# Kernel tuning notes

Measured on AMD Instinct MI355X. Metric: run time of the kernel, lower is better.

The kernel has to match this reference:

```python
import jax, jax.numpy as jnp
import numpy as np

TEMPERATURE = 8.0  # sqrt(d_k) with d_k = 64

def setup_inputs() -> dict:
    key = jax.random.key(0)
    kq, kk, kv = jax.random.split(key, 3)
    B, L, D = 16, 2048, 64  # heads, seq_len, head_dim
    q = jax.random.normal(kq, (B, L, D), dtype=jnp.float32)
    k = jax.random.normal(kk, (B, L, D), dtype=jnp.float32)
    v = jax.random.normal(kv, (B, L, D), dtype=jnp.float32)
    return {"q": q, "k": k, "v": v}

def reference(q, k, v):
    # scores: [B, Lq, Lk]
    scores = jnp.einsum('bqd,bkd->bqk', q, k) / TEMPERATURE
    log_attn = jax.nn.log_softmax(scores, axis=-1)
    attn = jnp.exp(log_attn)  # softmax, reusing the single stable reduction
    out = jnp.einsum('bqk,bkd->bqd', attn, v)        # [B, Lq, Dv]
    B, Lk, Dv = v.shape
    # transpose(0,1).reshape(Lk, Dv*B): heads folded into feature dim
    output = jnp.transpose(out, (1, 0, 2)).reshape(Lk, Dv * B)
    return (output, attn, log_attn)
```

## Files before the change

kernel.cpp:

```cpp
#include <hip/hip_runtime.h>

#define LSEQ 2048
#define NH   16
#define HD   64

typedef __attribute__((ext_vector_type(8))) short short8;
typedef __attribute__((ext_vector_type(4))) float f32x4;

__device__ __forceinline__ unsigned short f2b(float x) {
  unsigned int u = __builtin_bit_cast(unsigned int, x);
  u += 0x7FFFu + ((u >> 16) & 1u);
  return (unsigned short)(u >> 16);
}

__global__ __launch_bounds__(256) void prep_kernel(
    const float* __restrict__ q, const float* __restrict__ k, const float* __restrict__ v,
    unsigned short* __restrict__ qf, unsigned short* __restrict__ kf,
    unsigned short* __restrict__ vf) {
  const int b = blockIdx.y, lt = blockIdx.x;
  const int t = threadIdx.x;
  __shared__ unsigned short qls[64][80];
  __shared__ unsigned short kls[64][80];
  __shared__ float vls[64][65];
  const int l0 = lt * 64;

  #pragma unroll
  for (int i = 0; i < 2; ++i) {
    int c = t + i * 256;
    int r = c >> 3, d0 = (c & 7) * 8;
    size_t base = ((size_t)(b * LSEQ + l0 + r)) * HD + d0;
    float4 qa = *(const float4*)(q + base);
    float4 qc = *(const float4*)(q + base + 4);
    float4 ka = *(const float4*)(k + base);
    float4 kc = *(const float4*)(k + base + 4);
    float4 va = *(const float4*)(v + base);
    float4 vc = *(const float4*)(v + base + 4);
    qls[r][d0 + 0] = f2b(qa.x * 0.125f); qls[r][d0 + 1] = f2b(qa.y * 0.125f);
    qls[r][d0 + 2] = f2b(qa.z * 0.125f); qls[r][d0 + 3] = f2b(qa.w * 0.125f);
    qls[r][d0 + 4] = f2b(qc.x * 0.125f); qls[r][d0 + 5] = f2b(qc.y * 0.125f);
    qls[r][d0 + 6] = f2b(qc.z * 0.125f); qls[r][d0 + 7] = f2b(qc.w * 0.125f);
    kls[r][d0 + 0] = f2b(ka.x); kls[r][d0 + 1] = f2b(ka.y);
    kls[r][d0 + 2] = f2b(ka.z); kls[r][d0 + 3] = f2b(ka.w);
    kls[r][d0 + 4] = f2b(kc.x); kls[r][d0 + 5] = f2b(kc.y);
    kls[r][d0 + 6] = f2b(kc.z); kls[r][d0 + 7] = f2b(kc.w);
    vls[r][d0 + 0] = va.x; vls[r][d0 + 1] = va.y;
    vls[r][d0 + 2] = va.z; vls[r][d0 + 3] = va.w;
    vls[r][d0 + 4] = vc.x; vls[r][d0 + 5] = vc.y;
    vls[r][d0 + 6] = vc.z; vls[r][d0 + 7] = vc.w;
  }
  __syncthreads();

  #pragma unroll
  for (int i = 0; i < 2; ++i) {
    int c = t + i * 256;
    int l16 = c & 15, quad = (c >> 4) & 3, kk = (c >> 6) & 1, bl4 = c >> 7;
    short8 qv = *(const short8*)(&qls[bl4 * 16 + l16][kk * 32 + quad * 8]);
    short8 kv = *(const short8*)(&kls[bl4 * 16 + l16][kk * 32 + quad * 8]);
    size_t dst = ((((size_t)b * 128 + lt * 4 + bl4) * 2 + kk) * 64 + quad * 16 + l16) * 8;
    *(short8*)(qf + dst) = qv;
    *(short8*)(kf + dst) = kv;
    short8 vv8;
    #pragma unroll
    for (int j = 0; j < 8; ++j)
      vv8[j] = (short)f2b(vls[kk * 32 + quad * 8 + j][bl4 * 16 + l16]);
    size_t dstv = ((((size_t)b * 32 + lt) * 8 + bl4 * 2 + kk) * 64 + quad * 16 + l16) * 8;
    *(short8*)(vf + dstv) = vv8;
  }
}

__global__ __launch_bounds__(256) void attn_kernel(
    const unsigned short* __restrict__ qf, const unsigned short* __restrict__ kf,
    const unsigned short* __restrict__ vf,
    float* __restrict__ out0, float* __restrict__ attn, float* __restrict__ logp) {
  const int b = blockIdx.y, qt = blockIdx.x;
  const int t = threadIdx.x;
  const int w = t >> 6, lane = t & 63, quad = lane >> 4, l16 = lane & 15;
  __shared__ unsigned short ps[4][16][72];

  const int q0 = qt * 64;
  const int qrl = quad * 4;

  const size_t qbase = (((size_t)b * 128 + qt * 4 + w) * 2 * 64 + lane) * 8;
  short8 aq0 = *(const short8*)(qf + qbase);
  short8 aq1 = *(const short8*)(qf + qbase + 512);

  const unsigned short* kfb = kf + (size_t)b * 128 * 2 * 64 * 8;
  const unsigned short* vfb = vf + (size_t)b * 32 * 8 * 64 * 8;

  float p0 = 0.f, p1 = 0.f, p2 = 0.f, p3 = 0.f;
  for (int kt = 0; kt < 32; ++kt) {
    #pragma unroll
    for (int nt = 0; nt < 4; ++nt) {
      const unsigned short* kp = kfb + ((size_t)(kt * 4 + nt) * 128 + lane) * 8;
      short8 b0 = *(const short8*)(kp);
      short8 b1 = *(const short8*)(kp + 512);
      f32x4 s = {0.f, 0.f, 0.f, 0.f};
      s = __builtin_amdgcn_mfma_f32_16x16x32_bf16(aq0, b0, s, 0, 0, 0);
      s = __builtin_amdgcn_mfma_f32_16x16x32_bf16(aq1, b1, s, 0, 0, 0);
      p0 += __expf(s[0]); p1 += __expf(s[1]);
      p2 += __expf(s[2]); p3 += __expf(s[3]);
    }
  }
  #pragma unroll
  for (int off = 1; off < 16; off <<= 1) {
    p0 += __shfl_xor(p0, off, 64);
    p1 += __shfl_xor(p1, off, 64);
    p2 += __shfl_xor(p2, off, 64);
    p3 += __shfl_xor(p3, off, 64);
  }
  const float logl0 = __logf(p0), logl1 = __logf(p1);
  const float logl2 = __logf(p2), logl3 = __logf(p3);

  f32x4 oacc[4] = {{0.f,0.f,0.f,0.f},{0.f,0.f,0.f,0.f},{0.f,0.f,0.f,0.f},{0.f,0.f,0.f,0.f}};
  const size_t arow0 = ((size_t)(b * LSEQ + q0 + w * 16 + qrl)) * LSEQ;

  for (int kt = 0; kt < 32; ++kt) {
    #pragma unroll
    for (int nt = 0; nt < 4; ++nt) {
      const unsigned short* kp = kfb + ((size_t)(kt * 4 + nt) * 128 + lane) * 8;
      short8 b0 = *(const short8*)(kp);
      short8 b1 = *(const short8*)(kp + 512);
      f32x4 s = {0.f, 0.f, 0.f, 0.f};
      s = __builtin_amdgcn_mfma_f32_16x16x32_bf16(aq0, b0, s, 0, 0, 0);
      s = __builtin_amdgcn_mfma_f32_16x16x32_bf16(aq1, b1, s, 0, 0, 0);
      const int col = kt * 64 + nt * 16 + l16;
      const float la0 = s[0] - logl0; const float a0 = __expf(la0);
      const float la1 = s[1] - logl1; const float a1 = __expf(la1);
      const float la2 = s[2] - logl2; const float a2 = __expf(la2);
      const float la3 = s[3] - logl3; const float a3 = __expf(la3);
      attn[arow0 + col]            = a0;  logp[arow0 + col]            = la0;
      attn[arow0 + LSEQ + col]     = a1;  logp[arow0 + LSEQ + col]     = la1;
      attn[arow0 + 2 * LSEQ + col] = a2;  logp[arow0 + 2 * LSEQ + col] = la2;
      attn[arow0 + 3 * LSEQ + col] = a3;  logp[arow0 + 3 * LSEQ + col] = la3;
      ps[w][qrl + 0][nt * 16 + l16] = f2b(a0);
      ps[w][qrl + 1][nt * 16 + l16] = f2b(a1);
      ps[w][qrl + 2][nt * 16 + l16] = f2b(a2);
      ps[w][qrl + 3][nt * 16 + l16] = f2b(a3);
    }
    asm volatile("s_waitcnt lgkmcnt(0)" ::: "memory");
    short8 ap0 = *(const short8*)(&ps[w][l16][quad * 8]);
    short8 ap1 = *(const short8*)(&ps[w][l16][32 + quad * 8]);
    #pragma unroll
    for (int nt = 0; nt < 4; ++nt) {
      const unsigned short* vp = vfb + ((size_t)(kt * 8 + nt * 2) * 64 + lane) * 8;
      short8 v0 = *(const short8*)(vp);
      short8 v1 = *(const short8*)(vp + 512);
      oacc[nt] = __builtin_amdgcn_mfma_f32_16x16x32_bf16(ap0, v0, oacc[nt], 0, 0, 0);
      oacc[nt] = __builtin_amdgcn_mfma_f32_16x16x32_bf16(ap1, v1, oacc[nt], 0, 0, 0);
    }
    asm volatile("s_waitcnt lgkmcnt(0)" ::: "memory");
  }

  #pragma unroll
  for (int nt = 0; nt < 4; ++nt) {
    #pragma unroll
    for (int r = 0; r < 4; ++r) {
      out0[((size_t)(q0 + w * 16 + qrl + r)) * (NH * HD) + b * HD + nt * 16 + l16] =
          oacc[nt][r];
    }
  }
}

extern "C" void kernel_launch(void* const* d_in, const int* in_sizes, int n_in,
                              void* d_out, int out_size, void* d_ws, size_t ws_size,
                              hipStream_t stream) {
  const float* q = (const float*)d_in[0];
  const float* k = (const float*)d_in[1];
  const float* v = (const float*)d_in[2];
  float* out0 = (float*)d_out;
  float* attn = out0 + (size_t)LSEQ * NH * HD;
  float* logp = attn + (size_t)NH * LSEQ * LSEQ;

  unsigned short* qf = (unsigned short*)d_ws;
  unsigned short* kf = qf + (size_t)NH * LSEQ * HD;
  unsigned short* vf = kf + (size_t)NH * LSEQ * HD;

  dim3 grid(LSEQ / 64, NH);
  prep_kernel<<<grid, 256, 0, stream>>>(q, k, v, qf, kf, vf);
  attn_kernel<<<grid, 256, 0, stream>>>(qf, kf, vf, out0, attn, logp);
}
```

Measured before the change: 642.5 us.

## Split key dimension across blocks with partial denominators and atomic output accumulation

The attention kernel is split along the key dimension into four chunks. A separate denominator kernel computes per-chunk partial softmax sums, and the main kernel adds them before writing its slice of attn/logp. Each chunk accumulates its P·V contribution into the output with float atomics, and the prep kernel zeroes that output first. This raises the grid from 512 to 2048 blocks to improve occupancy on the many CUs, at the cost of an extra launch, recomputing QK in two kernels, and nondeterministic atomic summation.

```diff
diff --git a/kernel.cpp b/kernel.cpp
--- a/kernel.cpp
+++ b/kernel.cpp
@@ -3,6 +3,8 @@
 #define LSEQ 2048
 #define NH   16
 #define HD   64
+#define KSPLIT 4
+#define KT_PER 8
 
 typedef __attribute__((ext_vector_type(8))) short short8;
 typedef __attribute__((ext_vector_type(4))) float f32x4;
@@ -16,13 +18,20 @@
 __global__ __launch_bounds__(256) void prep_kernel(
     const float* __restrict__ q, const float* __restrict__ k, const float* __restrict__ v,
     unsigned short* __restrict__ qf, unsigned short* __restrict__ kf,
-    unsigned short* __restrict__ vf) {
+    unsigned short* __restrict__ vf, float* __restrict__ out0) {
   const int b = blockIdx.y, lt = blockIdx.x;
   const int t = threadIdx.x;
   __shared__ unsigned short qls[64][80];
   __shared__ unsigned short kls[64][80];
   __shared__ float vls[64][65];
   const int l0 = lt * 64;
+
+  {
+    float4 z = {0.f, 0.f, 0.f, 0.f};
+    size_t zbase = (((size_t)b * 32 + lt) * 256 + t) * 16;
+    #pragma unroll
+    for (int i = 0; i < 4; ++i) *(float4*)(out0 + zbase + i * 4) = z;
+  }
 
   #pragma unroll
   for (int i = 0; i < 2; ++i) {
@@ -68,27 +77,22 @@
   }
 }
 
-__global__ __launch_bounds__(256) void attn_kernel(
+__global__ __launch_bounds__(256, 4) void denom_kernel(
     const unsigned short* __restrict__ qf, const unsigned short* __restrict__ kf,
-    const unsigned short* __restrict__ vf,
-    float* __restrict__ out0, float* __restrict__ attn, float* __restrict__ logp) {
-  const int b = blockIdx.y, qt = blockIdx.x;
+    float* __restrict__ l_part) {
+  const int b = blockIdx.y, qt = blockIdx.x, ks = blockIdx.z;
   const int t = threadIdx.x;
   const int w = t >> 6, lane = t & 63, quad = lane >> 4, l16 = lane & 15;
-  __shared__ unsigned short ps[4][16][72];
-
   const int q0 = qt * 64;
-  const int qrl = quad * 4;
 
   const size_t qbase = (((size_t)b * 128 + qt * 4 + w) * 2 * 64 + lane) * 8;
   short8 aq0 = *(const short8*)(qf + qbase);
   short8 aq1 = *(const short8*)(qf + qbase + 512);
-
   const unsigned short* kfb = kf + (size_t)b * 128 * 2 * 64 * 8;
-  const unsigned short* vfb = vf + (size_t)b * 32 * 8 * 64 * 8;
 
   float p0 = 0.f, p1 = 0.f, p2 = 0.f, p3 = 0.f;
-  for (int kt = 0; kt < 32; ++kt) {
+  const int kt0 = ks * KT_PER;
+  for (int kt = kt0; kt < kt0 + KT_PER; ++kt) {
     #pragma unroll
     for (int nt = 0; nt < 4; ++nt) {
       const unsigned short* kp = kfb + ((size_t)(kt * 4 + nt) * 128 + lane) * 8;
@@ -108,13 +112,45 @@
     p2 += __shfl_xor(p2, off, 64);
     p3 += __shfl_xor(p3, off, 64);
   }
-  const float logl0 = __logf(p0), logl1 = __logf(p1);
-  const float logl2 = __logf(p2), logl3 = __logf(p3);
+  if (l16 == 0) {
+    float* lp = l_part + ((size_t)(ks * NH + b) * LSEQ) + q0 + w * 16 + quad * 4;
+    lp[0] = p0; lp[1] = p1; lp[2] = p2; lp[3] = p3;
+  }
+}
+
+__global__ __launch_bounds__(256, 4) void attn_kernel(
+    const unsigned short* __restrict__ qf, const unsigned short* __restrict__ kf,
+    const unsigned short* __restrict__ vf, const float* __restrict__ l_part,
+    float* __restrict__ out0, float* __restrict__ attn, float* __restrict__ logp) {
+  const int b = blockIdx.y, qt = blockIdx.x, ks = blockIdx.z;
+  const int t = threadIdx.x;
+  const int w = t >> 6, lane = t & 63, quad = lane >> 4, l16 = lane & 15;
+  __shared__ unsigned short ps[4][16][72];
+
+  const int q0 = qt * 64;
+  const int qrl = quad * 4;
+
+  const size_t qbase = (((size_t)b * 128 + qt * 4 + w) * 2 * 64 + lane) * 8;
+  short8 aq0 = *(const short8*)(qf + qbase);
+  short8 aq1 = *(const short8*)(qf + qbase + 512);
+
+  const unsigned short* kfb = kf + (size_t)b * 128 * 2 * 64 * 8;
+  const unsigned short* vfb = vf + (size_t)b * 32 * 8 * 64 * 8;
+
+  float ls0 = 0.f, ls1 = 0.f, ls2 = 0.f, ls3 = 0.f;
+  #pragma unroll
+  for (int s2 = 0; s2 < KSPLIT; ++s2) {
+    const float* lp = l_part + ((size_t)(s2 * NH + b) * LSEQ) + q0 + w * 16 + qrl;
+    ls0 += lp[0]; ls1 += lp[1]; ls2 += lp[2]; ls3 += lp[3];
+  }
+  const float logl0 = __logf(ls0), logl1 = __logf(ls1);
+  const float logl2 = __logf(ls2), logl3 = __logf(ls3);
 
   f32x4 oacc[4] = {{0.f,0.f,0.f,0.f},{0.f,0.f,0.f,0.f},{0.f,0.f,0.f,0.f},{0.f,0.f,0.f,0.f}};
   const size_t arow0 = ((size_t)(b * LSEQ + q0 + w * 16 + qrl)) * LSEQ;
 
-  for (int kt = 0; kt < 32; ++kt) {
+  const int kt0 = ks * KT_PER;
+  for (int kt = kt0; kt < kt0 + KT_PER; ++kt) {
     #pragma unroll
     for (int nt = 0; nt < 4; ++nt) {
       const unsigned short* kp = kfb + ((size_t)(kt * 4 + nt) * 128 + lane) * 8;
@@ -155,8 +191,8 @@
   for (int nt = 0; nt < 4; ++nt) {
     #pragma unroll
     for (int r = 0; r < 4; ++r) {
-      out0[((size_t)(q0 + w * 16 + qrl + r)) * (NH * HD) + b * HD + nt * 16 + l16] =
-          oacc[nt][r];
+      atomicAdd(&out0[((size_t)(q0 + w * 16 + qrl + r)) * (NH * HD) + b * HD + nt * 16 + l16],
+                oacc[nt][r]);
     }
   }
 }
@@ -174,8 +210,11 @@
   unsigned short* qf = (unsigned short*)d_ws;
   unsigned short* kf = qf + (size_t)NH * LSEQ * HD;
   unsigned short* vf = kf + (size_t)NH * LSEQ * HD;
+  float* l_part = (float*)(vf + (size_t)NH * LSEQ * HD);
 
   dim3 grid(LSEQ / 64, NH);
-  prep_kernel<<<grid, 256, 0, stream>>>(q, k, v, qf, kf, vf);
-  attn_kernel<<<grid, 256, 0, stream>>>(qf, kf, vf, out0, attn, logp);
-}
+  prep_kernel<<<grid, 256, 0, stream>>>(q, k, v, qf, kf, vf, out0);
+  dim3 gridk(LSEQ / 64, NH, KSPLIT);
+  denom_kernel<<<gridk, 256, 0, stream>>>(qf, kf, l_part);
+  attn_kernel<<<gridk, 256, 0, stream>>>(qf, kf, vf, l_part, out0, attn, logp);
+}
```

Result: no change. 636.1 us (-1.0%).
